# Performance work log

Measured on AMD Instinct MI355X. Metric: run time of the kernel, lower is better.

The kernel has to match this reference:

```python
import jax, jax.numpy as jnp
import numpy as np

EMB = 384
H = 6
D = 64
B = 256
T = 256


def setup_inputs() -> dict:
    key = jax.random.key(0)
    ks = jax.random.split(key, 6)
    s = 1.0 / np.sqrt(EMB)
    return {
        "x": jax.random.normal(ks[0], (B, T, EMB), dtype=jnp.float32),
        "wq": jax.random.normal(ks[1], (H, EMB, D), dtype=jnp.float32) * s,
        "wk": jax.random.normal(ks[2], (H, EMB, D), dtype=jnp.float32) * s,
        "wv": jax.random.normal(ks[3], (H, EMB, D), dtype=jnp.float32) * s,
        "w_proj": jax.random.normal(ks[4], (H * D, EMB), dtype=jnp.float32) * s,
        "b_proj": jax.random.normal(ks[5], (EMB,), dtype=jnp.float32) * 0.01,
    }


def reference(x, wq, wk, wv, w_proj, b_proj):
    # x: [B, T, E]; per-head projections stacked over H (dropout in eval mode)
    q = jnp.einsum("bte,hed->bhtd", x, wq)
    k = jnp.einsum("bte,hed->bhtd", x, wk)
    v = jnp.einsum("bte,hed->bhtd", x, wv)
    scale = q.shape[-1] ** -0.5
    scores = jnp.einsum("bhqd,bhkd->bhqk", q, k) * scale  # [B,H,T,T]
    tq = q.shape[2]
    causal = jnp.tril(jnp.ones((tq, tq), dtype=bool))
    scores = jnp.where(causal, scores, -jnp.inf)
    att = jax.nn.softmax(scores, axis=-1)
    out = jnp.einsum("bhqk,bhkd->bhqd", att, v)  # [B,H,T,D]
    out = out.transpose(0, 2, 1, 3).reshape(x.shape[0], tq, -1)  # concat heads
    return out @ w_proj + b_proj
```

## Files before the change

### kernel.cpp

```cpp
#include <hip/hip_runtime.h>
#include <hip/hip_bf16.h>


#define Bn 256
#define Tn 256
#define En 384
#define Hn 6
#define Dn 64

typedef __bf16 bf16x8 __attribute__((ext_vector_type(8)));
typedef float f32x4 __attribute__((ext_vector_type(4)));
typedef unsigned short u16x8 __attribute__((ext_vector_type(8)));

static __device__ __forceinline__ unsigned short f2bf(float f) {
    unsigned int u = __builtin_bit_cast(unsigned int, f);
    u += 0x7fffu + ((u >> 16) & 1u);
    return (unsigned short)(u >> 16);
}

static __device__ __forceinline__ f32x4 mfma16(bf16x8 a, bf16x8 b, f32x4 c) {
    return __builtin_amdgcn_mfma_f32_16x16x32_bf16(a, b, c, 0, 0, 0);
}

static __device__ __forceinline__ void glds16(const unsigned short* g, unsigned short* l) {
    __builtin_amdgcn_global_load_lds(
        (const __attribute__((address_space(1))) unsigned int*)g,
        (__attribute__((address_space(3))) unsigned int*)l, 16, 0, 0);
}

__global__ __launch_bounds__(256) void prep_kernel(
    const float* __restrict__ wq, const float* __restrict__ wk,
    const float* __restrict__ wv, const float* __restrict__ wp,
    unsigned short* __restrict__ wt, unsigned short* __restrict__ wpt) {
    const int NW = 3 * Hn * Dn * En;
    const int NP = En * En;
    int idx = blockIdx.x * 256 + threadIdx.x;
    if (idx < NW) {
        int e = idx % En;
        int d = (idx / En) % Dn;
        int h = (idx / (En * Dn)) % Hn;
        int t = idx / (En * Dn * Hn);
        const float* src = (t == 0) ? wq : (t == 1) ? wk : wv;
        wt[idx] = f2bf(src[(h * En + e) * Dn + d]);
    } else if (idx < NW + NP) {
        int j = idx - NW;
        int k = j % En;
        int n = j / En;
        wpt[j] = f2bf(wp[k * En + n]);
    }
}

__global__ __launch_bounds__(256) void xcast_kernel(
    const float* __restrict__ x, unsigned short* __restrict__ xb) {
    size_t i = ((size_t)blockIdx.x * 256 + threadIdx.x) * 8;
    float4 f0 = *(const float4*)(x + i);
    float4 f1 = *(const float4*)(x + i + 4);
    u16x8 p;
    p[0] = f2bf(f0.x); p[1] = f2bf(f0.y); p[2] = f2bf(f0.z); p[3] = f2bf(f0.w);
    p[4] = f2bf(f1.x); p[5] = f2bf(f1.y); p[6] = f2bf(f1.z); p[7] = f2bf(f1.w);
    *(u16x8*)(xb + i) = p;
}

__global__ __launch_bounds__(256) void qkv_gemm(
    const unsigned short* __restrict__ xb, const unsigned short* __restrict__ wt,
    unsigned short* __restrict__ Qo, unsigned short* __restrict__ Ko,
    unsigned short* __restrict__ Vt) {
    __shared__ unsigned short As[2][128][64];
    __shared__ unsigned short Bs[2][192][64];

    const int h = blockIdx.x;
    const int m0 = blockIdx.y * 128;

    const int tid = threadIdx.x;
    const int wave = tid >> 6, lane = tid & 63;
    const int quad = lane >> 4, l16 = lane & 15;
    const int mw = (wave >> 1) * 64, nw = (wave & 1) * 96;

    f32x4 acc[4][6];
#pragma unroll
    for (int i = 0; i < 4; ++i)
#pragma unroll
        for (int j = 0; j < 6; ++j) acc[i][j] = (f32x4){0.f, 0.f, 0.f, 0.f};

    const int lr = lane >> 3;
    const int js = (lane & 7) ^ lr;

    const unsigned short* ga[4];
#pragma unroll
    for (int i = 0; i < 4; ++i)
        ga[i] = xb + (size_t)(m0 + wave * 32 + i * 8 + lr) * En + js * 8;
    const unsigned short* gb[6];
#pragma unroll
    for (int i = 0; i < 6; ++i) {
        int n = wave * 48 + i * 8 + lr;
        gb[i] = wt + (size_t)(((n >> 6) * Hn + h) * Dn + (n & 63)) * En + js * 8;
    }

#define QKV_STAGE(buf, koff)                                              \
    do {                                                                  \
        _Pragma("unroll") for (int i = 0; i < 4; ++i)                     \
            glds16(ga[i] + (koff), &As[buf][wave * 32 + i * 8][0]);       \
        _Pragma("unroll") for (int i = 0; i < 6; ++i)                     \
            glds16(gb[i] + (koff), &Bs[buf][wave * 48 + i * 8][0]);       \
    } while (0)

    QKV_STAGE(0, 0);
    __syncthreads();

    int cur = 0;
    for (int kb = 0; kb < 6; ++kb) {
        if (kb < 5) QKV_STAGE(cur ^ 1, (kb + 1) * 64);

#pragma unroll
        for (int ks = 0; ks < 2; ++ks) {
            bf16x8 a[4], b[6];
            const int ps = ((ks * 4 + quad) ^ (l16 & 7)) * 8;
#pragma unroll
            for (int mi = 0; mi < 4; ++mi)
                a[mi] = *(const bf16x8*)&As[cur][mw + mi * 16 + l16][ps];
#pragma unroll
            for (int ni = 0; ni < 6; ++ni)
                b[ni] = *(const bf16x8*)&Bs[cur][nw + ni * 16 + l16][ps];
#pragma unroll
            for (int mi = 0; mi < 4; ++mi)
#pragma unroll
                for (int ni = 0; ni < 6; ++ni) acc[mi][ni] = mfma16(a[mi], b[ni], acc[mi][ni]);
        }
        if (kb < 5) {
            __syncthreads();
            cur ^= 1;
        }
    }
#undef QKV_STAGE

    const int b = m0 >> 8, tbase = m0 & 255;
    unsigned short* qkbase[2] = {
        Qo + (size_t)((b * Hn + h) * Tn) * Dn,
        Ko + (size_t)((b * Hn + h) * Tn) * Dn };
    unsigned short* vdst = Vt + (size_t)((b * Hn + h) * Dn) * Tn;
#pragma unroll
    for (int ni = 0; ni < 6; ++ni) {
        const int ng = nw + ni * 16;
        const int tensor = ng >> 6;
        const int d = (ng & 63) + l16;
        if (tensor < 2) {
            unsigned short* dst = qkbase[tensor];
#pragma unroll
            for (int mi = 0; mi < 4; ++mi)
#pragma unroll
                for (int r = 0; r < 4; ++r) {
                    int t = tbase + mw + mi * 16 + quad * 4 + r;
                    dst[t * Dn + d] = f2bf(acc[mi][ni][r]);
                }
        } else {
#pragma unroll
            for (int mi = 0; mi < 4; ++mi) {
                int t0 = tbase + mw + mi * 16 + quad * 4;
                ushort4 pk;
                pk.x = f2bf(acc[mi][ni][0]);
                pk.y = f2bf(acc[mi][ni][1]);
                pk.z = f2bf(acc[mi][ni][2]);
                pk.w = f2bf(acc[mi][ni][3]);
                *(ushort4*)&vdst[d * Tn + t0] = pk;
            }
        }
    }
}

__global__ __launch_bounds__(256) void attn_kernel(
    const unsigned short* __restrict__ Q, const unsigned short* __restrict__ K,
    const unsigned short* __restrict__ Vt, unsigned short* __restrict__ attout) {
    __shared__ unsigned short Kt[64][72];
    __shared__ unsigned short Vl[64][72];
    __shared__ unsigned short P[64][72];

    const int qt = blockIdx.x, h = blockIdx.y, b = blockIdx.z;
    const int q0 = qt * 64;
    const unsigned short* Qb = Q + (size_t)((b * Hn + h) * Tn) * Dn;
    const unsigned short* Kb = K + (size_t)((b * Hn + h) * Tn) * Dn;
    const unsigned short* Vb = Vt + (size_t)((b * Hn + h) * Dn) * Tn;

    const int tid = threadIdx.x;
    const int wave = tid >> 6, lane = tid & 63;
    const int quad = lane >> 4, l16 = lane & 15;

    bf16x8 aq[2];
#pragma unroll
    for (int ks = 0; ks < 2; ++ks)
        aq[ks] = *(const bf16x8*)&Qb[(q0 + wave * 16 + l16) * Dn + ks * 32 + quad * 8];

    f32x4 O[4];
#pragma unroll
    for (int i = 0; i < 4; ++i) O[i] = (f32x4){0.f, 0.f, 0.f, 0.f};
    float rsum[4] = {0.f, 0.f, 0.f, 0.f};

    const int sr = tid >> 2, sc = (tid & 3) * 16;
    const int qrow_base = q0 + wave * 16 + quad * 4;
    const float cexp = 0.125f * 1.44269504f;

#pragma unroll
    for (int kt = 0; kt < 4; ++kt) {
        if (kt <= qt) {
            __syncthreads();
            const unsigned short* kr = Kb + (kt * 64 + sr) * Dn + sc;
            *(uint4*)&Kt[sr][sc] = *(const uint4*)kr;
            *(uint4*)&Kt[sr][sc + 8] = *(const uint4*)(kr + 8);
            const unsigned short* vr = Vb + sr * Tn + kt * 64 + sc;
            *(uint4*)&Vl[sr][sc] = *(const uint4*)vr;
            *(uint4*)&Vl[sr][sc + 8] = *(const uint4*)(vr + 8);
            __syncthreads();

            f32x4 S[4];
#pragma unroll
            for (int i = 0; i < 4; ++i) S[i] = (f32x4){0.f, 0.f, 0.f, 0.f};
#pragma unroll
            for (int ks = 0; ks < 2; ++ks)
#pragma unroll
                for (int ni = 0; ni < 4; ++ni) {
                    bf16x8 bk = *(const bf16x8*)&Kt[ni * 16 + l16][ks * 32 + quad * 8];
                    S[ni] = mfma16(aq[ks], bk, S[ni]);
                }

#pragma unroll
            for (int ni = 0; ni < 4; ++ni)
#pragma unroll
                for (int r = 0; r < 4; ++r) {
                    int col = kt * 64 + ni * 16 + l16;
                    float p = exp2f(S[ni][r] * cexp);
                    p = (col > qrow_base + r) ? 0.f : p;
                    rsum[r] += p;
                    P[wave * 16 + quad * 4 + r][ni * 16 + l16] = f2bf(p);
                }

#pragma unroll
            for (int ks = 0; ks < 2; ++ks) {
                bf16x8 ap = *(const bf16x8*)&P[wave * 16 + l16][ks * 32 + quad * 8];
#pragma unroll
                for (int ni = 0; ni < 4; ++ni) {
                    bf16x8 bv = *(const bf16x8*)&Vl[ni * 16 + l16][ks * 32 + quad * 8];
                    O[ni] = mfma16(ap, bv, O[ni]);
                }
            }
        }
    }

#pragma unroll
    for (int r = 0; r < 4; ++r) {
        float s = rsum[r];
        s += __shfl_xor(s, 1);
        s += __shfl_xor(s, 2);
        s += __shfl_xor(s, 4);
        s += __shfl_xor(s, 8);
        rsum[r] = s;
    }

    __syncthreads();
#pragma unroll
    for (int r = 0; r < 4; ++r) {
        float inv = 1.0f / rsum[r];
#pragma unroll
        for (int ni = 0; ni < 4; ++ni)
            Kt[wave * 16 + quad * 4 + r][ni * 16 + l16] = f2bf(O[ni][r] * inv);
    }
    __syncthreads();
    const int row = tid >> 2;
    const int col = (tid & 3) * 16;
    unsigned short* dst = attout + (size_t)(b * Tn + q0 + row) * (Hn * Dn) + h * Dn + col;
    *(uint4*)dst = *(const uint4*)&Kt[row][col];
    *(uint4*)(dst + 8) = *(const uint4*)&Kt[row][col + 8];
}

__global__ __launch_bounds__(256) void proj_gemm(
    const unsigned short* __restrict__ attout, const unsigned short* __restrict__ wpt,
    const float* __restrict__ bproj, float* __restrict__ out) {
    __shared__ unsigned short As[2][128][64];
    __shared__ unsigned short Bs[2][128][64];

    const int n0 = blockIdx.x * 128;
    const int m0 = blockIdx.y * 128;

    const int tid = threadIdx.x;
    const int wave = tid >> 6, lane = tid & 63;
    const int quad = lane >> 4, l16 = lane & 15;
    const int mw = (wave >> 1) * 64, nw = (wave & 1) * 64;

    f32x4 acc[4][4];
#pragma unroll
    for (int i = 0; i < 4; ++i)
#pragma unroll
        for (int j = 0; j < 4; ++j) acc[i][j] = (f32x4){0.f, 0.f, 0.f, 0.f};

    const int lr = lane >> 3;
    const int js = (lane & 7) ^ lr;

    const unsigned short* ga[4];
    const unsigned short* gb[4];
#pragma unroll
    for (int i = 0; i < 4; ++i) {
        ga[i] = attout + (size_t)(m0 + wave * 32 + i * 8 + lr) * En + js * 8;
        gb[i] = wpt + (size_t)(n0 + wave * 32 + i * 8 + lr) * En + js * 8;
    }

#define PROJ_STAGE(buf, koff)                                             \
    do {                                                                  \
        _Pragma("unroll") for (int i = 0; i < 4; ++i)                     \
            glds16(ga[i] + (koff), &As[buf][wave * 32 + i * 8][0]);       \
        _Pragma("unroll") for (int i = 0; i < 4; ++i)                     \
            glds16(gb[i] + (koff), &Bs[buf][wave * 32 + i * 8][0]);       \
    } while (0)

    PROJ_STAGE(0, 0);
    __syncthreads();

    int cur = 0;
    for (int kb = 0; kb < 6; ++kb) {
        if (kb < 5) PROJ_STAGE(cur ^ 1, (kb + 1) * 64);

#pragma unroll
        for (int ks = 0; ks < 2; ++ks) {
            bf16x8 a[4], bb[4];
            const int ps = ((ks * 4 + quad) ^ (l16 & 7)) * 8;
#pragma unroll
            for (int mi = 0; mi < 4; ++mi)
                a[mi] = *(const bf16x8*)&As[cur][mw + mi * 16 + l16][ps];
#pragma unroll
            for (int ni = 0; ni < 4; ++ni)
                bb[ni] = *(const bf16x8*)&Bs[cur][nw + ni * 16 + l16][ps];
#pragma unroll
            for (int mi = 0; mi < 4; ++mi)
#pragma unroll
                for (int ni = 0; ni < 4; ++ni) acc[mi][ni] = mfma16(a[mi], bb[ni], acc[mi][ni]);
        }
        if (kb < 5) {
            __syncthreads();
            cur ^= 1;
        }
    }
#undef PROJ_STAGE

#pragma unroll
    for (int mi = 0; mi < 4; ++mi)
#pragma unroll
        for (int ni = 0; ni < 4; ++ni)
#pragma unroll
            for (int r = 0; r < 4; ++r) {
                int row = m0 + mw + mi * 16 + quad * 4 + r;
                int col = n0 + nw + ni * 16 + l16;
                out[(size_t)row * En + col] = acc[mi][ni][r] + bproj[col];
            }
}

extern "C" void kernel_launch(void* const* d_in, const int* in_sizes, int n_in,
                              void* d_out, int out_size, void* d_ws, size_t ws_size,
                              hipStream_t stream) {
    const float* x  = (const float*)d_in[0];
    const float* wq = (const float*)d_in[1];
    const float* wk = (const float*)d_in[2];
    const float* wv = (const float*)d_in[3];
    const float* wp = (const float*)d_in[4];
    const float* bp = (const float*)d_in[5];
    float* out = (float*)d_out;

    char* ws = (char*)d_ws;
    const size_t WT_OFF  = 0;
    const size_t WPT_OFF = WT_OFF + 884736;
    const size_t Q_OFF   = WPT_OFF + 294912;
    const size_t K_OFF   = Q_OFF + 50331648ull;
    const size_t VT_OFF  = K_OFF + 50331648ull;
    const size_t XB_OFF  = VT_OFF + 50331648ull;

    unsigned short* wt   = (unsigned short*)(ws + WT_OFF);
    unsigned short* wpt  = (unsigned short*)(ws + WPT_OFF);
    unsigned short* Qd   = (unsigned short*)(ws + Q_OFF);
    unsigned short* Kd   = (unsigned short*)(ws + K_OFF);
    unsigned short* Vtd  = (unsigned short*)(ws + VT_OFF);
    unsigned short* xbd  = (unsigned short*)(ws + XB_OFF);
    unsigned short* ao   = xbd;

    prep_kernel<<<2304, 256, 0, stream>>>(wq, wk, wv, wp, wt, wpt);
    xcast_kernel<<<12288, 256, 0, stream>>>(x, xbd);
    qkv_gemm<<<dim3(Hn, 512), 256, 0, stream>>>(xbd, wt, Qd, Kd, Vtd);
    attn_kernel<<<dim3(4, Hn, Bn), 256, 0, stream>>>(Qd, Kd, Vtd, ao);
    proj_gemm<<<dim3(3, 512), 256, 0, stream>>>(ao, wpt, bp, out);
}
```

Before: 387.3 us.

## Process whole (batch, head) per block with full K/V in shared memory

The attention kernel now launches one block per (head, batch) instead of one per 64-row query tile. It loads all of K and V^T into XOR-swizzled shared memory once via direct global-to-LDS copies, then has each wave handle four 16-row query groups paired for causal load balance. This removes redundant K/V reloads across query tiles and the per-tile block barriers. In exchange, shared memory per block grows to about 73 KB, which may reduce occupancy, and the grid shrinks by a factor of four.

After: 379.4 us. 2.0% less time.

```diff
diff --git a/kernel.cpp b/kernel.cpp
--- a/kernel.cpp
+++ b/kernel.cpp
@@ -170,12 +170,11 @@
 __global__ __launch_bounds__(256) void attn_kernel(
     const unsigned short* __restrict__ Q, const unsigned short* __restrict__ K,
     const unsigned short* __restrict__ Vt, unsigned short* __restrict__ attout) {
-    __shared__ unsigned short Kt[64][72];
-    __shared__ unsigned short Vl[64][72];
-    __shared__ unsigned short P[64][72];
-
-    const int qt = blockIdx.x, h = blockIdx.y, b = blockIdx.z;
-    const int q0 = qt * 64;
+    __shared__ unsigned short Kt[256][64];
+    __shared__ unsigned short Vl[64][256];
+    __shared__ unsigned short P[4][16][72];
+
+    const int h = blockIdx.x, b = blockIdx.y;
     const unsigned short* Qb = Q + (size_t)((b * Hn + h) * Tn) * Dn;
     const unsigned short* Kb = K + (size_t)((b * Hn + h) * Tn) * Dn;
     const unsigned short* Vb = Vt + (size_t)((b * Hn + h) * Dn) * Tn;
@@ -184,32 +183,42 @@
     const int wave = tid >> 6, lane = tid & 63;
     const int quad = lane >> 4, l16 = lane & 15;
 
-    bf16x8 aq[2];
-#pragma unroll
-    for (int ks = 0; ks < 2; ++ks)
-        aq[ks] = *(const bf16x8*)&Qb[(q0 + wave * 16 + l16) * Dn + ks * 32 + quad * 8];
-
-    f32x4 O[4];
-#pragma unroll
-    for (int i = 0; i < 4; ++i) O[i] = (f32x4){0.f, 0.f, 0.f, 0.f};
-    float rsum[4] = {0.f, 0.f, 0.f, 0.f};
-
-    const int sr = tid >> 2, sc = (tid & 3) * 16;
-    const int qrow_base = q0 + wave * 16 + quad * 4;
+    {
+        const unsigned short* kg = Kb + (size_t)(lane >> 3) * Dn + ((lane & 7) ^ (lane >> 3)) * 8;
+#pragma unroll
+        for (int i = 0; i < 8; ++i) {
+            const int c = wave * 8 + i;
+            glds16(kg + (size_t)c * 8 * Dn, &Kt[c * 8][0]);
+        }
+#pragma unroll
+        for (int i = 0; i < 8; ++i) {
+            const int c = wave * 8 + i;
+            const int d = c * 2 + (lane >> 5);
+            const int j = (lane & 31) ^ (d & 7);
+            glds16(Vb + (size_t)d * Tn + j * 8, &Vl[c * 2][0]);
+        }
+    }
+    __syncthreads();
+
     const float cexp = 0.125f * 1.44269504f;
-
-#pragma unroll
-    for (int kt = 0; kt < 4; ++kt) {
-        if (kt <= qt) {
-            __syncthreads();
-            const unsigned short* kr = Kb + (kt * 64 + sr) * Dn + sc;
-            *(uint4*)&Kt[sr][sc] = *(const uint4*)kr;
-            *(uint4*)&Kt[sr][sc + 8] = *(const uint4*)(kr + 8);
-            const unsigned short* vr = Vb + sr * Tn + kt * 64 + sc;
-            *(uint4*)&Vl[sr][sc] = *(const uint4*)vr;
-            *(uint4*)&Vl[sr][sc + 8] = *(const uint4*)(vr + 8);
-            __syncthreads();
-
+    const int grp[4] = {wave, 7 - wave, 8 + wave, 15 - wave};
+
+    for (int gi = 0; gi < 4; ++gi) {
+        const int g = grp[gi];
+        const int q0 = g * 16;
+
+        bf16x8 aq[2];
+#pragma unroll
+        for (int ks = 0; ks < 2; ++ks)
+            aq[ks] = *(const bf16x8*)&Qb[(q0 + l16) * Dn + ks * 32 + quad * 8];
+
+        f32x4 O[4];
+#pragma unroll
+        for (int i = 0; i < 4; ++i) O[i] = (f32x4){0.f, 0.f, 0.f, 0.f};
+        float rsum[4] = {0.f, 0.f, 0.f, 0.f};
+
+        const int ktmax = g >> 2;
+        for (int kt = 0; kt <= ktmax; ++kt) {
             f32x4 S[4];
 #pragma unroll
             for (int i = 0; i < 4; ++i) S[i] = (f32x4){0.f, 0.f, 0.f, 0.f};
@@ -217,7 +226,8 @@
             for (int ks = 0; ks < 2; ++ks)
 #pragma unroll
                 for (int ni = 0; ni < 4; ++ni) {
-                    bf16x8 bk = *(const bf16x8*)&Kt[ni * 16 + l16][ks * 32 + quad * 8];
+                    bf16x8 bk = *(const bf16x8*)
+                        &Kt[kt * 64 + ni * 16 + l16][(((ks * 4 + quad) ^ (l16 & 7)) * 8)];
                     S[ni] = mfma16(aq[ks], bk, S[ni]);
                 }
 
@@ -227,47 +237,46 @@
                 for (int r = 0; r < 4; ++r) {
                     int col = kt * 64 + ni * 16 + l16;
                     float p = exp2f(S[ni][r] * cexp);
-                    p = (col > qrow_base + r) ? 0.f : p;
+                    p = (col > q0 + quad * 4 + r) ? 0.f : p;
                     rsum[r] += p;
-                    P[wave * 16 + quad * 4 + r][ni * 16 + l16] = f2bf(p);
+                    P[wave][quad * 4 + r][ni * 16 + l16] = f2bf(p);
                 }
 
 #pragma unroll
             for (int ks = 0; ks < 2; ++ks) {
-                bf16x8 ap = *(const bf16x8*)&P[wave * 16 + l16][ks * 32 + quad * 8];
+                bf16x8 ap = *(const bf16x8*)&P[wave][l16][ks * 32 + quad * 8];
 #pragma unroll
                 for (int ni = 0; ni < 4; ++ni) {
-                    bf16x8 bv = *(const bf16x8*)&Vl[ni * 16 + l16][ks * 32 + quad * 8];
+                    bf16x8 bv = *(const bf16x8*)
+                        &Vl[ni * 16 + l16][(((kt * 8 + ks * 4 + quad) ^ (l16 & 7)) * 8)];
                     O[ni] = mfma16(ap, bv, O[ni]);
                 }
             }
         }
-    }
-
-#pragma unroll
-    for (int r = 0; r < 4; ++r) {
-        float s = rsum[r];
-        s += __shfl_xor(s, 1);
-        s += __shfl_xor(s, 2);
-        s += __shfl_xor(s, 4);
-        s += __shfl_xor(s, 8);
-        rsum[r] = s;
-    }
-
-    __syncthreads();
-#pragma unroll
-    for (int r = 0; r < 4; ++r) {
-        float inv = 1.0f / rsum[r];
-#pragma unroll
-        for (int ni = 0; ni < 4; ++ni)
-            Kt[wave * 16 + quad * 4 + r][ni * 16 + l16] = f2bf(O[ni][r] * inv);
-    }
-    __syncthreads();
-    const int row = tid >> 2;
-    const int col = (tid & 3) * 16;
-    unsigned short* dst = attout + (size_t)(b * Tn + q0 + row) * (Hn * Dn) + h * Dn + col;
-    *(uint4*)dst = *(const uint4*)&Kt[row][col];
-    *(uint4*)(dst + 8) = *(const uint4*)&Kt[row][col + 8];
+
+#pragma unroll
+        for (int r = 0; r < 4; ++r) {
+            float s = rsum[r];
+            s += __shfl_xor(s, 1);
+            s += __shfl_xor(s, 2);
+            s += __shfl_xor(s, 4);
+            s += __shfl_xor(s, 8);
+            rsum[r] = s;
+        }
+
+#pragma unroll
+        for (int r = 0; r < 4; ++r) {
+            float inv = 1.0f / rsum[r];
+#pragma unroll
+            for (int ni = 0; ni < 4; ++ni)
+                P[wave][quad * 4 + r][ni * 16 + l16] = f2bf(O[ni][r] * inv);
+        }
+        const int row = lane >> 2;
+        const int colc = (lane & 3) * 16;
+        unsigned short* dst = attout + (size_t)(b * Tn + q0 + row) * (Hn * Dn) + h * Dn + colc;
+        *(uint4*)dst = *(const uint4*)&P[wave][row][colc];
+        *(uint4*)(dst + 8) = *(const uint4*)&P[wave][row][colc + 8];
+    }
 }
 
 __global__ __launch_bounds__(256) void proj_gemm(
@@ -380,6 +389,6 @@
     prep_kernel<<<2304, 256, 0, stream>>>(wq, wk, wv, wp, wt, wpt);
     xcast_kernel<<<12288, 256, 0, stream>>>(x, xbd);
     qkv_gemm<<<dim3(Hn, 512), 256, 0, stream>>>(xbd, wt, Qd, Kd, Vtd);
-    attn_kernel<<<dim3(4, Hn, Bn), 256, 0, stream>>>(Qd, Kd, Vtd, ao);
+    attn_kernel<<<dim3(Hn, Bn), 256, 0, stream>>>(Qd, Kd, Vtd, ao);
     proj_gemm<<<dim3(3, 512), 256, 0, stream>>>(ao, wpt, bp, out);
 }
```
